# Optimization experiments

Hardware: AMD Instinct MI355X
Metric: run time of the kernel (lower is better)

The kernel has to match this reference:

```python
import jax, jax.numpy as jnp
import numpy as np

B, T, H = 16, 64, 256  # batch, timesteps (= num stacked layers), hidden
L = T                  # MultiRNNCell([cell]*timesteps): layers == timesteps, shared weights


def setup_inputs() -> dict:
    key = jax.random.key(0)
    k1, k2, k3 = jax.random.split(key, 3)
    x = jax.random.normal(k1, (B, T, H), dtype=jnp.float32)
    init_state = jax.random.normal(k2, (L, 2, B, H), dtype=jnp.float32) * 0.1  # [L, (c,h), B, H]
    W = jax.random.normal(k3, (2 * H, 4 * H), dtype=jnp.float32) / np.sqrt(2 * H)
    b = jnp.zeros((4 * H,), dtype=jnp.float32)
    return {"x": x, "init_state": init_state, "W": W, "b": b}


def reference(x, init_state, W, b):
    # TF LSTMCell math: gates order (i, j, f, o), forget_bias = 1.0
    c0 = init_state[:, 0]  # [L,B,H]
    h0 = init_state[:, 1]  # [L,B,H]

    def layer_fn(inp, st):
        # inp: [B,H] input to this layer; st = (c,h) each [B,H]
        lc, lh = st
        z = jnp.concatenate([inp, lh], axis=-1) @ W + b  # [B,4H]
        i, j, f, o = jnp.split(z, 4, axis=-1)
        nc = jax.nn.sigmoid(f + 1.0) * lc + jax.nn.sigmoid(i) * jnp.tanh(j)
        nh = jax.nn.sigmoid(o) * jnp.tanh(nc)
        return nh, (nc, nh)  # carry = input to next layer; ys = new per-layer state

    def step(carry, xt):
        # carry: (c,h) each [L,B,H]; xt: [B,H]
        c, h = carry
        top_h, (nc, nh) = jax.lax.scan(layer_fn, xt, (c, h))
        return (nc, nh), top_h

    (_, _), ys = jax.lax.scan(step, (c0, h0), jnp.transpose(x, (1, 0, 2)))  # ys: [T,B,H]
    return jnp.transpose(ys, (1, 0, 2))  # [B,T,H] top-layer outputs (dynamic_rnn outputs)
```

## Files before the change

kernel.cpp:

```cpp
#include <hip/hip_runtime.h>

typedef _Float16 half8 __attribute__((ext_vector_type(8)));
typedef float f32x4 __attribute__((ext_vector_type(4)));

#define SCOPE __HIP_MEMORY_SCOPE_AGENT

constexpr size_t OFF_FLAGS = 0;
constexpr size_t OFF_H     = 65536;

__device__ __forceinline__ size_t Hidx(int slot, int l, int b, int u) {
  return (((size_t)slot * 64 + l) * 16 + b) * 256 + u;
}
__device__ __forceinline__ float sigm(float v) { return 1.0f / (1.0f + __expf(-v)); }
__device__ __forceinline__ float tanh_(float v) { return 1.0f - 2.0f / (__expf(2.0f * v) + 1.0f); }

__global__ void init_ws(const float* __restrict__ init_state, char* ws) {
  int* flags = (int*)(ws + OFF_FLAGS);
  _Float16* Hp = (_Float16*)(ws + OFF_H);
  const int tid = blockIdx.x * 256 + threadIdx.x;
  if (tid < 4096) flags[tid] = 0;
  for (int e = tid; e < 64 * 16 * 256; e += 65536) {
    const int u = e & 255, b = (e >> 8) & 15, l = e >> 12;
    Hp[Hidx(1, l, b, u)] = (_Float16)init_state[((l * 2 + 1) * 16 + b) * 256 + u];
  }
}

__device__ __forceinline__ void spin_ge4(int* p) {
  for (int it = 0; it < 4000000; ++it) {
    if (__hip_atomic_load(p, __ATOMIC_RELAXED, SCOPE) >= 4) return;
    __builtin_amdgcn_s_sleep(1);
  }
}

__global__ __launch_bounds__(256, 1) void lstm_mfma(
    const float* __restrict__ x, const float* __restrict__ init_state,
    const float* __restrict__ W, const float* __restrict__ bias,
    float* __restrict__ out, char* ws) {
  int* flags = (int*)(ws + OFF_FLAGS);
  unsigned long long* Hp64 = (unsigned long long*)(ws + OFF_H);

  const int tid = threadIdx.x;
  const int wg = blockIdx.x;
  const int l = wg >> 2, r = wg & 3;
  const int wv = tid >> 6, lane = tid & 63;

  __shared__ alignas(16) _Float16 aLds[16 * 64 * 8];
  __shared__ alignas(16) float zLds[16 * 260];
  __shared__ unsigned short hLds[16 * 64];

  half8 wreg[64];
#pragma unroll
  for (int q = 0; q < 4; ++q) {
    const int nl = (wv * 4 + q) * 16 + (lane & 15);
    const int col = (nl & 3) * 256 + r * 64 + (nl >> 2);
#pragma unroll
    for (int kb = 0; kb < 16; ++kb) {
      const int k0 = kb * 32 + (lane >> 4) * 8;
      const float* src = W + (size_t)k0 * 1024 + col;
      half8 hv;
#pragma unroll
      for (int jj = 0; jj < 8; ++jj) hv[jj] = (_Float16)src[(size_t)jj * 1024];
      wreg[q * 16 + kb] = hv;
    }
  }

  const int hu = tid & 63, b4 = tid >> 6;
  const int gu = r * 64 + hu;
  float creg[4];
#pragma unroll
  for (int bi = 0; bi < 4; ++bi)
    creg[bi] = init_state[((l * 2 + 0) * 16 + (b4 * 4 + bi)) * 256 + gu];
  const float bi_ = bias[0 * 256 + gu], bj_ = bias[1 * 256 + gu];
  const float bf_ = bias[2 * 256 + gu], bo_ = bias[3 * 256 + gu];

  for (int t = 0; t < 64; ++t) {
    const int slotCur = t & 1, slotPrev = (t + 1) & 1;

    if (tid == 0) {
      if (l > 0) spin_ge4(&flags[(l - 1) * 64 + t]);
      if (t > 0) spin_ge4(&flags[l * 64 + (t - 1)]);
      if (t >= 2 && l < 63) spin_ge4(&flags[(l + 1) * 64 + (t - 2)]);
    }
    __syncthreads();

#pragma unroll
    for (int i = 0; i < 4; ++i) {
      const int e = i * 256 + tid;
      const int kb = e >> 6, ln = e & 63;
      const int m = ln & 15, k0 = kb * 32 + (ln >> 4) * 8;
      _Float16* dst = &aLds[(size_t)(kb * 64 + ln) * 8];
      if (kb < 8) {
        if (l == 0) {
          const float* xs = x + ((size_t)m * 64 + t) * 256 + k0;
          half8 hv;
#pragma unroll
          for (int jj = 0; jj < 8; ++jj) hv[jj] = (_Float16)xs[jj];
          *(half8*)dst = hv;
        } else {
          const size_t b64 = Hidx(slotCur, l - 1, m, k0) >> 2;
          unsigned long long a0 = __hip_atomic_load(Hp64 + b64, __ATOMIC_RELAXED, SCOPE);
          unsigned long long a1 = __hip_atomic_load(Hp64 + b64 + 1, __ATOMIC_RELAXED, SCOPE);
          ((unsigned long long*)dst)[0] = a0;
          ((unsigned long long*)dst)[1] = a1;
        }
      } else {
        const size_t b64 = Hidx(slotPrev, l, m, k0 - 256) >> 2;
        unsigned long long a0 = __hip_atomic_load(Hp64 + b64, __ATOMIC_RELAXED, SCOPE);
        unsigned long long a1 = __hip_atomic_load(Hp64 + b64 + 1, __ATOMIC_RELAXED, SCOPE);
        ((unsigned long long*)dst)[0] = a0;
        ((unsigned long long*)dst)[1] = a1;
      }
    }
    __syncthreads();

    f32x4 acc[4] = {{0.f, 0.f, 0.f, 0.f}, {0.f, 0.f, 0.f, 0.f},
                    {0.f, 0.f, 0.f, 0.f}, {0.f, 0.f, 0.f, 0.f}};
#pragma unroll
    for (int kb = 0; kb < 16; ++kb) {
      half8 a = *(const half8*)&aLds[(kb * 64 + lane) * 8];
#pragma unroll
      for (int q = 0; q < 4; ++q)
        acc[q] = __builtin_amdgcn_mfma_f32_16x16x32_f16(a, wreg[q * 16 + kb], acc[q], 0, 0, 0);
    }

#pragma unroll
    for (int q = 0; q < 4; ++q) {
      const int nl = (wv * 4 + q) * 16 + (lane & 15);
      const int m0 = (lane >> 4) * 4;
#pragma unroll
      for (int rg = 0; rg < 4; ++rg) zLds[(m0 + rg) * 260 + nl] = acc[q][rg];
    }
    __syncthreads();

#pragma unroll
    for (int bi = 0; bi < 4; ++bi) {
      const int b = b4 * 4 + bi;
      f32x4 zg = *(const f32x4*)&zLds[b * 260 + hu * 4];
      const float iv = zg[0] + bi_, jv = zg[1] + bj_;
      const float fv = zg[2] + bf_, ov = zg[3] + bo_;
      const float nc = sigm(fv + 1.0f) * creg[bi] + sigm(iv) * tanh_(jv);
      const float nh = sigm(ov) * tanh_(nc);
      creg[bi] = nc;
      union { _Float16 f; unsigned short s; } cv;
      cv.f = (_Float16)nh;
      hLds[b * 64 + hu] = cv.s;
      if (l == 63) out[((size_t)b * 64 + t) * 256 + gu] = nh;
    }
    __syncthreads();

    {
      const int b = tid >> 4, u0 = (tid & 15) * 4;
      unsigned long long v = *(unsigned long long*)&hLds[b * 64 + u0];
      __hip_atomic_store(Hp64 + (Hidx(slotCur, l, b, r * 64 + u0) >> 2), v,
                         __ATOMIC_RELAXED, SCOPE);
    }
    __syncthreads();
    if (tid == 0)
      __hip_atomic_fetch_add(&flags[l * 64 + t], 1, __ATOMIC_RELEASE, SCOPE);
  }
}

extern "C" void kernel_launch(void* const* d_in, const int* in_sizes, int n_in,
                              void* d_out, int out_size, void* d_ws,
                              size_t ws_size, hipStream_t stream) {
  const float* x          = (const float*)d_in[0];
  const float* init_state = (const float*)d_in[1];
  const float* W          = (const float*)d_in[2];
  const float* bias       = (const float*)d_in[3];
  float* out = (float*)d_out;
  char* ws   = (char*)d_ws;

  init_ws<<<256, 256, 0, stream>>>(init_state, ws);
  lstm_mfma<<<256, 256, 0, stream>>>(x, init_state, W, bias, out, ws);
}
```

Measured before the change: 786.5 us.

## Use per-workgroup monotonic flags, load A fragments directly to registers, defer backpressure wait

```diff
diff --git a/kernel.cpp b/kernel.cpp
--- a/kernel.cpp
+++ b/kernel.cpp
@@ -1,7 +1,9 @@
 #include <hip/hip_runtime.h>
 
 typedef _Float16 half8 __attribute__((ext_vector_type(8)));
+typedef _Float16 half4 __attribute__((ext_vector_type(4)));
 typedef float f32x4 __attribute__((ext_vector_type(4)));
+typedef unsigned long long ull;
 
 #define SCOPE __HIP_MEMORY_SCOPE_AGENT
 
@@ -25,102 +27,131 @@
   }
 }
 
-__device__ __forceinline__ void spin_ge4(int* p) {
-  for (int it = 0; it < 4000000; ++it) {
-    if (__hip_atomic_load(p, __ATOMIC_RELAXED, SCOPE) >= 4) return;
-    __builtin_amdgcn_s_sleep(1);
-  }
-}
-
 __global__ __launch_bounds__(256, 1) void lstm_mfma(
     const float* __restrict__ x, const float* __restrict__ init_state,
     const float* __restrict__ W, const float* __restrict__ bias,
     float* __restrict__ out, char* ws) {
   int* flags = (int*)(ws + OFF_FLAGS);
-  unsigned long long* Hp64 = (unsigned long long*)(ws + OFF_H);
+  ull* fl64 = (ull*)flags;
+  ull* Hp64 = (ull*)(ws + OFF_H);
 
   const int tid = threadIdx.x;
   const int wg = blockIdx.x;
   const int l = wg >> 2, r = wg & 3;
   const int wv = tid >> 6, lane = tid & 63;
-
-  __shared__ alignas(16) _Float16 aLds[16 * 64 * 8];
-  __shared__ alignas(16) float zLds[16 * 260];
-  __shared__ unsigned short hLds[16 * 64];
+  const int m = lane & 15, ksub = (lane >> 4) * 8;
+
+  __shared__ alignas(16) float smemRaw[32 * 257];
+  float* wstage = smemRaw;
+  float* zLds = smemRaw;
 
   half8 wreg[64];
-#pragma unroll
-  for (int q = 0; q < 4; ++q) {
-    const int nl = (wv * 4 + q) * 16 + (lane & 15);
-    const int col = (nl & 3) * 256 + r * 64 + (nl >> 2);
-#pragma unroll
-    for (int kb = 0; kb < 16; ++kb) {
-      const int k0 = kb * 32 + (lane >> 4) * 8;
-      const float* src = W + (size_t)k0 * 1024 + col;
+  for (int c = 0; c < 16; ++c) {
+    const float* Wc = W + (size_t)(c * 32) * 1024 + (tid >> 6) * 256 + r * 64 + (tid & 63);
+#pragma unroll
+    for (int rr = 0; rr < 32; ++rr)
+      wstage[rr * 257 + tid] = Wc[(size_t)rr * 1024];
+    __syncthreads();
+#pragma unroll
+    for (int q = 0; q < 4; ++q) {
+      const int nl = (wv * 4 + q) * 16 + (lane & 15);
+      const int pos = (nl & 3) * 64 + (nl >> 2);
       half8 hv;
 #pragma unroll
-      for (int jj = 0; jj < 8; ++jj) hv[jj] = (_Float16)src[(size_t)jj * 1024];
-      wreg[q * 16 + kb] = hv;
-    }
+      for (int jj = 0; jj < 8; ++jj)
+        hv[jj] = (_Float16)wstage[(ksub + jj) * 257 + pos];
+      wreg[q * 16 + c] = hv;
+    }
+    __syncthreads();
   }
 
-  const int hu = tid & 63, b4 = tid >> 6;
-  const int gu = r * 64 + hu;
-  float creg[4];
-#pragma unroll
-  for (int bi = 0; bi < 4; ++bi)
-    creg[bi] = init_state[((l * 2 + 0) * 16 + (b4 * 4 + bi)) * 256 + gu];
-  const float bi_ = bias[0 * 256 + gu], bj_ = bias[1 * 256 + gu];
-  const float bf_ = bias[2 * 256 + gu], bo_ = bias[3 * 256 + gu];
+  const int eb = tid >> 4;
+  const int ju = (tid & 15) * 4;
+  const int gu0 = r * 64 + ju;
+  f32x4 creg = *(const f32x4*)(init_state + ((l * 2 + 0) * 16 + eb) * 256 + gu0);
+  const f32x4 bI = *(const f32x4*)(bias + 0 * 256 + gu0);
+  const f32x4 bJ = *(const f32x4*)(bias + 1 * 256 + gu0);
+  const f32x4 bF = *(const f32x4*)(bias + 2 * 256 + gu0);
+  const f32x4 bO = *(const f32x4*)(bias + 3 * 256 + gu0);
 
   for (int t = 0; t < 64; ++t) {
     const int slotCur = t & 1, slotPrev = (t + 1) & 1;
 
-    if (tid == 0) {
-      if (l > 0) spin_ge4(&flags[(l - 1) * 64 + t]);
-      if (t > 0) spin_ge4(&flags[l * 64 + (t - 1)]);
-      if (t >= 2 && l < 63) spin_ge4(&flags[(l + 1) * 64 + (t - 2)]);
-    }
-    __syncthreads();
-
-#pragma unroll
-    for (int i = 0; i < 4; ++i) {
-      const int e = i * 256 + tid;
-      const int kb = e >> 6, ln = e & 63;
-      const int m = ln & 15, k0 = kb * 32 + (ln >> 4) * 8;
-      _Float16* dst = &aLds[(size_t)(kb * 64 + ln) * 8];
-      if (kb < 8) {
-        if (l == 0) {
-          const float* xs = x + ((size_t)m * 64 + t) * 256 + k0;
-          half8 hv;
-#pragma unroll
-          for (int jj = 0; jj < 8; ++jj) hv[jj] = (_Float16)xs[jj];
-          *(half8*)dst = hv;
-        } else {
-          const size_t b64 = Hidx(slotCur, l - 1, m, k0) >> 2;
-          unsigned long long a0 = __hip_atomic_load(Hp64 + b64, __ATOMIC_RELAXED, SCOPE);
-          unsigned long long a1 = __hip_atomic_load(Hp64 + b64 + 1, __ATOMIC_RELAXED, SCOPE);
-          ((unsigned long long*)dst)[0] = a0;
-          ((unsigned long long*)dst)[1] = a1;
-        }
-      } else {
-        const size_t b64 = Hidx(slotPrev, l, m, k0 - 256) >> 2;
-        unsigned long long a0 = __hip_atomic_load(Hp64 + b64, __ATOMIC_RELAXED, SCOPE);
-        unsigned long long a1 = __hip_atomic_load(Hp64 + b64 + 1, __ATOMIC_RELAXED, SCOPE);
-        ((unsigned long long*)dst)[0] = a0;
-        ((unsigned long long*)dst)[1] = a1;
-      }
-    }
-    __syncthreads();
+    if (l > 0 || t > 0) {
+      const int pi = (l - 1) * 2, si = l * 2;
+      for (int it = 0; it < (1 << 22); ++it) {
+        bool ok = true;
+        if (l > 0) {
+          ull p0 = __hip_atomic_load(fl64 + pi, __ATOMIC_RELAXED, SCOPE);
+          ull p1 = __hip_atomic_load(fl64 + pi + 1, __ATOMIC_RELAXED, SCOPE);
+          const int need = t + 1;
+          ok &= ((int)p0 >= need) & ((int)(p0 >> 32) >= need) &
+                ((int)p1 >= need) & ((int)(p1 >> 32) >= need);
+        }
+        if (t > 0) {
+          ull s0 = __hip_atomic_load(fl64 + si, __ATOMIC_RELAXED, SCOPE);
+          ull s1 = __hip_atomic_load(fl64 + si + 1, __ATOMIC_RELAXED, SCOPE);
+          ok &= ((int)s0 >= t) & ((int)(s0 >> 32) >= t) &
+                ((int)s1 >= t) & ((int)(s1 >> 32) >= t);
+        }
+        if (ok) break;
+        __builtin_amdgcn_s_sleep(1);
+      }
+    }
+
+    const bool bpNeed = (l < 63) && (t >= 2);
+    ull bp0 = 0, bp1 = 0;
+    if (bpNeed) {
+      bp0 = __hip_atomic_load(fl64 + (l + 1) * 2, __ATOMIC_RELAXED, SCOPE);
+      bp1 = __hip_atomic_load(fl64 + (l + 1) * 2 + 1, __ATOMIC_RELAXED, SCOPE);
+    }
+
+    half8 afrag[16];
+    if (l == 0) {
+      const float* xb = x + ((size_t)m * 64 + t) * 256;
+#pragma unroll
+      for (int kb = 0; kb < 8; ++kb) {
+        const int k0 = kb * 32 + ksub;
+        f32x4 x0 = *(const f32x4*)(xb + k0);
+        f32x4 x1 = *(const f32x4*)(xb + k0 + 4);
+        half8 hv;
+#pragma unroll
+        for (int jj = 0; jj < 4; ++jj) {
+          hv[jj] = (_Float16)x0[jj];
+          hv[4 + jj] = (_Float16)x1[jj];
+        }
+        afrag[kb] = hv;
+      }
+    } else {
+#pragma unroll
+      for (int kb = 0; kb < 8; ++kb) {
+        const size_t o = Hidx(slotCur, l - 1, m, kb * 32 + ksub) >> 2;
+        ull a0 = __hip_atomic_load(Hp64 + o, __ATOMIC_RELAXED, SCOPE);
+        ull a1 = __hip_atomic_load(Hp64 + o + 1, __ATOMIC_RELAXED, SCOPE);
+        half8 hv;
+        ((ull*)&hv)[0] = a0;
+        ((ull*)&hv)[1] = a1;
+        afrag[kb] = hv;
+      }
+    }
+#pragma unroll
+    for (int kb = 8; kb < 16; ++kb) {
+      const size_t o = Hidx(slotPrev, l, m, (kb - 8) * 32 + ksub) >> 2;
+      ull a0 = __hip_atomic_load(Hp64 + o, __ATOMIC_RELAXED, SCOPE);
+      ull a1 = __hip_atomic_load(Hp64 + o + 1, __ATOMIC_RELAXED, SCOPE);
+      half8 hv;
+      ((ull*)&hv)[0] = a0;
+      ((ull*)&hv)[1] = a1;
+      afrag[kb] = hv;
+    }
 
     f32x4 acc[4] = {{0.f, 0.f, 0.f, 0.f}, {0.f, 0.f, 0.f, 0.f},
                     {0.f, 0.f, 0.f, 0.f}, {0.f, 0.f, 0.f, 0.f}};
 #pragma unroll
     for (int kb = 0; kb < 16; ++kb) {
-      half8 a = *(const half8*)&aLds[(kb * 64 + lane) * 8];
 #pragma unroll
       for (int q = 0; q < 4; ++q)
-        acc[q] = __builtin_amdgcn_mfma_f32_16x16x32_f16(a, wreg[q * 16 + kb], acc[q], 0, 0, 0);
+        acc[q] = __builtin_amdgcn_mfma_f32_16x16x32_f16(afrag[kb], wreg[q * 16 + kb], acc[q], 0, 0, 0);
     }
 
 #pragma unroll
@@ -132,31 +163,51 @@
     }
     __syncthreads();
 
-#pragma unroll
-    for (int bi = 0; bi < 4; ++bi) {
-      const int b = b4 * 4 + bi;
-      f32x4 zg = *(const f32x4*)&zLds[b * 260 + hu * 4];
-      const float iv = zg[0] + bi_, jv = zg[1] + bj_;
-      const float fv = zg[2] + bf_, ov = zg[3] + bo_;
-      const float nc = sigm(fv + 1.0f) * creg[bi] + sigm(iv) * tanh_(jv);
+    if (bpNeed) {
+      const int need = t - 1;
+      bool ok = ((int)bp0 >= need) & ((int)(bp0 >> 32) >= need) &
+                ((int)bp1 >= need) & ((int)(bp1 >> 32) >= need);
+      if (!ok) {
+        for (int it = 0; it < (1 << 22); ++it) {
+          bp0 = __hip_atomic_load(fl64 + (l + 1) * 2, __ATOMIC_RELAXED, SCOPE);
+          bp1 = __hip_atomic_load(fl64 + (l + 1) * 2 + 1, __ATOMIC_RELAXED, SCOPE);
+          ok = ((int)bp0 >= need) & ((int)(bp0 >> 32) >= need) &
+               ((int)bp1 >= need) & ((int)(bp1 >> 32) >= need);
+          if (ok) break;
+          __builtin_amdgcn_s_sleep(1);
+        }
+      }
+    }
+
+    const float* zb = &zLds[eb * 260 + ju * 4];
+    f32x4 zz[4];
+    zz[0] = *(const f32x4*)(zb + 0);
+    zz[1] = *(const f32x4*)(zb + 4);
+    zz[2] = *(const f32x4*)(zb + 8);
+    zz[3] = *(const f32x4*)(zb + 12);
+    half4 nhv;
+    f32x4 outv;
+#pragma unroll
+    for (int jj = 0; jj < 4; ++jj) {
+      const float iv = zz[jj][0] + bI[jj];
+      const float jv = zz[jj][1] + bJ[jj];
+      const float fv = zz[jj][2] + bF[jj];
+      const float ov = zz[jj][3] + bO[jj];
+      const float nc = sigm(fv + 1.0f) * creg[jj] + sigm(iv) * tanh_(jv);
       const float nh = sigm(ov) * tanh_(nc);
-      creg[bi] = nc;
-      union { _Float16 f; unsigned short s; } cv;
-      cv.f = (_Float16)nh;
-      hLds[b * 64 + hu] = cv.s;
-      if (l == 63) out[((size_t)b * 64 + t) * 256 + gu] = nh;
-    }
-    __syncthreads();
-
-    {
-      const int b = tid >> 4, u0 = (tid & 15) * 4;
-      unsigned long long v = *(unsigned long long*)&hLds[b * 64 + u0];
-      __hip_atomic_store(Hp64 + (Hidx(slotCur, l, b, r * 64 + u0) >> 2), v,
-                         __ATOMIC_RELAXED, SCOPE);
-    }
-    __syncthreads();
+      creg[jj] = nc;
+      nhv[jj] = (_Float16)nh;
+      outv[jj] = nh;
+    }
+    union { half4 h; ull u; } pu;
+    pu.h = nhv;
+    __hip_atomic_store(Hp64 + (Hidx(slotCur, l, eb, gu0) >> 2), pu.u,
+                       __ATOMIC_RELAXED, SCOPE);
+    if (l == 63) *(f32x4*)(out + ((size_t)eb * 64 + t) * 256 + gu0) = outv;
+    __syncthreads();
+
     if (tid == 0)
-      __hip_atomic_fetch_add(&flags[l * 64 + t], 1, __ATOMIC_RELEASE, SCOPE);
+      __hip_atomic_store(&flags[l * 4 + r], t + 1, __ATOMIC_RELEASE, SCOPE);
   }
 }
 
```

New measurement: 2.307 ms. 2.93x slower.
